# Kernel optimization log

Hardware: AMD Instinct MI355X
Metric: run time of the kernel (lower is better)

The kernel has to match this reference:

```python
import jax, jax.numpy as jnp
import numpy as np

ALPHA = 0.2  # LeakyReLU negative slope


def setup_inputs() -> dict:
    key = jax.random.key(0)
    k1, k2, k3, k4 = jax.random.split(key, 4)
    B, N, F_in, F_out = 2, 512, 256, 128
    x = jax.random.normal(k1, (B, N, F_in), dtype=jnp.float32)
    adj = jax.random.randint(k2, (B, N, N), 0, 2, dtype=jnp.int32)
    # xavier_uniform with gain=1.414 for W (in_features, out_features)
    limit = 1.414 * np.sqrt(6.0 / (F_in + F_out))
    W = jax.random.uniform(k3, (F_in, F_out), dtype=jnp.float32, minval=-limit, maxval=limit)
    # attn_fc: Linear(out_features, 1, bias=False); store its weight as a vector
    lim_a = np.sqrt(1.0 / F_out)
    a_fc = jax.random.uniform(k4, (F_out,), dtype=jnp.float32, minval=-lim_a, maxval=lim_a)
    return {"x": x, "adj": adj, "W": W, "a_fc": a_fc}


def reference(x, adj, W, a_fc):
    # x: [B,N,F_in], adj: [B,N,N], W: [F_in,F_out], a_fc: [F_out]
    Wh = jnp.einsum('bnf,fo->bno', x, W)                         # [B,N,O]
    s = Wh[:, :, None, :] + Wh[:, None, :, :]                    # [B,N,N,O] broadcast concat-sum
    e = jnp.einsum('bijo,o->bij', jax.nn.leaky_relu(s, ALPHA), a_fc)  # attn_fc -> [B,N,N]
    e = e / jnp.sqrt(jnp.sum(e * e))                             # torch.linalg.norm over whole tensor
    e = jnp.where(adj == 0, -jnp.inf, e)
    attention = jax.nn.softmax(e, axis=-1)
    h_prime = jnp.einsum('bij,bjo->bio', attention, Wh)          # [B,N,O]
    return jax.nn.elu(h_prime)                                   # concat=True -> elu
```

## Files before the change

kernel.cpp:

```cpp
#include <hip/hip_runtime.h>
#include <math.h>

constexpr int BB   = 2;
constexpr int NN   = 512;
constexpr int FIN  = 256;
constexpr int FOUT = 128;

__global__ __launch_bounds__(512) void wh_u_kernel(const float* __restrict__ x,
                                                   const float* __restrict__ W,
                                                   const float* __restrict__ a_fc,
                                                   float* __restrict__ Wh,
                                                   float* __restrict__ u) {
    __shared__ float  xs[4][FIN];
    __shared__ float4 part[4][4][32];
    __shared__ float  upart[8][4];

    const int t  = threadIdx.x;
    const int g0 = blockIdx.x * 4;

    if (t < 256)
        ((float4*)xs)[t] = ((const float4*)(x + (size_t)g0 * FIN))[t];
    __syncthreads();

    const int rl = t >> 7;
    const int fs = (t >> 5) & 3;
    const int og = t & 31;
    const float* xr = &xs[rl][fs * 64];
    const float4* W4 = (const float4*)W;

    float4 acc = {0.f, 0.f, 0.f, 0.f};
#pragma unroll 8
    for (int f = 0; f < 64; ++f) {
        const float  xv = xr[f];
        const float4 wv = W4[(size_t)(fs * 64 + f) * 32 + og];
        acc.x = fmaf(xv, wv.x, acc.x);
        acc.y = fmaf(xv, wv.y, acc.y);
        acc.z = fmaf(xv, wv.z, acc.z);
        acc.w = fmaf(xv, wv.w, acc.w);
    }
    part[rl][fs][og] = acc;
    __syncthreads();

    if (t < 128) {
        const int crl = t & 3;
        const int cog = t >> 2;
        const float4 s0 = part[crl][0][cog];
        const float4 s1 = part[crl][1][cog];
        const float4 s2 = part[crl][2][cog];
        const float4 s3 = part[crl][3][cog];
        float4 w4;
        w4.x = (s0.x + s1.x) + (s2.x + s3.x);
        w4.y = (s0.y + s1.y) + (s2.y + s3.y);
        w4.z = (s0.z + s1.z) + (s2.z + s3.z);
        w4.w = (s0.w + s1.w) + (s2.w + s3.w);
        ((float4*)(Wh + (size_t)(g0 + crl) * FOUT))[cog] = w4;

        const float4 a4 = ((const float4*)a_fc)[cog];
        float pa = w4.x * a4.x + w4.y * a4.y + w4.z * a4.z + w4.w * a4.w;
#pragma unroll
        for (int off = 32; off >= 4; off >>= 1) pa += __shfl_down(pa, off);
        if ((t & 63) < 4) upart[t >> 6][t & 3] = pa;
    }
    __syncthreads();
    if (t < 4) {
        u[g0 + t] = upart[0][t] + upart[1][t];
    }
}

__global__ __launch_bounds__(256) void e_kernel(const float* __restrict__ Wh,
                                                const float* __restrict__ u,
                                                const float* __restrict__ a_fc,
                                                float* __restrict__ e_buf,
                                                float* __restrict__ partials) {
    __shared__ float whi[32][132];
    __shared__ float whj[16][132];
    __shared__ float a2[FOUT];
    __shared__ float usi[32];
    __shared__ float usj[16];
    __shared__ float parts[16][4][33];
    __shared__ float red[4];

    const int t   = threadIdx.x;
    const int bj0 = blockIdx.x * 16;
    const int bi0 = blockIdx.y * 32;
    const int b   = blockIdx.z;
    const float* whb = Wh + (size_t)(b * NN) * FOUT;

#pragma unroll
    for (int it = 0; it < 4; ++it) {
        const int idx = it * 256 + t;
        const int row = idx >> 5, c4 = idx & 31;
        *(float4*)&whi[row][c4 * 4] =
            *(const float4*)(whb + (size_t)(bi0 + row) * FOUT + c4 * 4);
    }
#pragma unroll
    for (int it = 0; it < 2; ++it) {
        const int idx = it * 256 + t;
        const int row = idx >> 5, c4 = idx & 31;
        *(float4*)&whj[row][c4 * 4] =
            *(const float4*)(whb + (size_t)(bj0 + row) * FOUT + c4 * 4);
    }
    if (t < 32)            usi[t]       = u[b * NN + bi0 + t];
    else if (t < 48)       usj[t - 32]  = u[b * NN + bj0 + (t - 32)];
    else if (t >= 128)     a2[t - 128]  = 0.4f * a_fc[t - 128];
    __syncthreads();

    const int w    = t >> 6;
    const int lane = t & 63;
    const int i    = lane & 31;
    const int jh   = lane >> 5;
    const int ob   = w * 32;

    float4 iv[8], av[8];
#pragma unroll
    for (int k = 0; k < 8; ++k) {
        iv[k] = *(const float4*)&whi[i][ob + 4 * k];
        av[k] = *(const float4*)&a2[ob + 4 * k];
    }

#pragma unroll
    for (int jj = 0; jj < 8; ++jj) {
        const int j = jh * 8 + jj;
        float4 acc = {0.f, 0.f, 0.f, 0.f};
#pragma unroll
        for (int k = 0; k < 8; ++k) {
            const float4 jv = *(const float4*)&whj[j][ob + 4 * k];
            float s;
            s = iv[k].x + jv.x; acc.x = fmaf(av[k].x, fabsf(s), acc.x);
            s = iv[k].y + jv.y; acc.y = fmaf(av[k].y, fabsf(s), acc.y);
            s = iv[k].z + jv.z; acc.z = fmaf(av[k].z, fabsf(s), acc.z);
            s = iv[k].w + jv.w; acc.w = fmaf(av[k].w, fabsf(s), acc.w);
        }
        parts[j][w][i] = (acc.x + acc.y) + (acc.z + acc.w);
    }
    __syncthreads();

    const int ci = t >> 3;
    const int jp = (t & 7) * 2;
    const float ui = usi[ci];

    const float S0 = (parts[jp][0][ci] + parts[jp][1][ci]) +
                     (parts[jp][2][ci] + parts[jp][3][ci]);
    const float v0 = fmaf(0.6f, ui + usj[jp], S0);
    const float S1 = (parts[jp + 1][0][ci] + parts[jp + 1][1][ci]) +
                     (parts[jp + 1][2][ci] + parts[jp + 1][3][ci]);
    const float v1 = fmaf(0.6f, ui + usj[jp + 1], S1);
    float ss = fmaf(v0, v0, v1 * v1);

    float2 e2 = {v0, v1};
    *(float2*)&e_buf[(size_t)(b * NN + bi0 + ci) * NN + bj0 + jp] = e2;

#pragma unroll
    for (int off = 32; off; off >>= 1) ss += __shfl_down(ss, off);
    if ((t & 63) == 0) red[t >> 6] = ss;
    __syncthreads();
    if (t == 0)
        partials[(blockIdx.z * 16 + blockIdx.y) * 32 + blockIdx.x] =
            (red[0] + red[1]) + (red[2] + red[3]);
}

__global__ __launch_bounds__(256) void softmax_pv_kernel(
        const float* __restrict__ e_buf, const int* __restrict__ adj,
        const float* __restrict__ Wh, const float* __restrict__ partials,
        float* __restrict__ out) {
    __shared__ float p[4][NN];
    __shared__ float hb[3][4][64];
    __shared__ float red[4];
    __shared__ float rsv[4];

    const int t    = threadIdx.x;
    const int w    = t >> 6;
    const int lane = t & 63;

    float v = (partials[t] + partials[t + 256]) +
              (partials[t + 512] + partials[t + 768]);
#pragma unroll
    for (int off = 32; off; off >>= 1) v += __shfl_down(v, off);
    if (lane == 0) red[w] = v;
    __syncthreads();
    const float inv_norm = 1.0f / sqrtf((red[0] + red[1]) + (red[2] + red[3]));

    const int g0  = (blockIdx.x & 255) * 4;
    const int row = g0 + w;

    const float4* er4 = (const float4*)(e_buf + (size_t)row * NN);
    const int4*   ad4 = (const int4*)(adj + (size_t)row * NN);
    const float4 ea = er4[lane],     eb = er4[lane + 64];
    const int4   aa = ad4[lane],     ab = ad4[lane + 64];

    float va[8];
    va[0] = aa.x ? ea.x * inv_norm : -INFINITY;
    va[1] = aa.y ? ea.y * inv_norm : -INFINITY;
    va[2] = aa.z ? ea.z * inv_norm : -INFINITY;
    va[3] = aa.w ? ea.w * inv_norm : -INFINITY;
    va[4] = ab.x ? eb.x * inv_norm : -INFINITY;
    va[5] = ab.y ? eb.y * inv_norm : -INFINITY;
    va[6] = ab.z ? eb.z * inv_norm : -INFINITY;
    va[7] = ab.w ? eb.w * inv_norm : -INFINITY;

    float mx = va[0];
#pragma unroll
    for (int c = 1; c < 8; ++c) mx = fmaxf(mx, va[c]);
#pragma unroll
    for (int off = 32; off; off >>= 1) mx = fmaxf(mx, __shfl_xor(mx, off));

    float pv[8], sum = 0.f;
#pragma unroll
    for (int c = 0; c < 8; ++c) { pv[c] = expf(va[c] - mx); sum += pv[c]; }
    float4 pa = {pv[0], pv[1], pv[2], pv[3]};
    float4 pb = {pv[4], pv[5], pv[6], pv[7]};
    ((float4*)&p[w][0])[lane]      = pa;
    ((float4*)&p[w][0])[lane + 64] = pb;

#pragma unroll
    for (int off = 32; off; off >>= 1) sum += __shfl_xor(sum, off);
    if (lane == 0) rsv[w] = 1.0f / sum;
    __syncthreads();

    const int oo = lane;
    const int o  = (blockIdx.x >> 8) * 64 + oo;
    const int b  = g0 >> 9;
    const float* whb = Wh + (size_t)(b * NN) * FOUT;
    const int j0 = w * 128;

    float acc[4] = {0.f, 0.f, 0.f, 0.f};
    for (int j = j0; j < j0 + 128; j += 4) {
        const float4 p0 = *(const float4*)&p[0][j];
        const float4 p1 = *(const float4*)&p[1][j];
        const float4 p2 = *(const float4*)&p[2][j];
        const float4 p3 = *(const float4*)&p[3][j];
        const float q0[4] = {p0.x, p0.y, p0.z, p0.w};
        const float q1[4] = {p1.x, p1.y, p1.z, p1.w};
        const float q2[4] = {p2.x, p2.y, p2.z, p2.w};
        const float q3[4] = {p3.x, p3.y, p3.z, p3.w};
#pragma unroll
        for (int q = 0; q < 4; ++q) {
            const float wv = whb[(size_t)(j + q) * FOUT + o];
            acc[0] = fmaf(q0[q], wv, acc[0]);
            acc[1] = fmaf(q1[q], wv, acc[1]);
            acc[2] = fmaf(q2[q], wv, acc[2]);
            acc[3] = fmaf(q3[q], wv, acc[3]);
        }
    }

    if (w) {
        hb[w - 1][0][oo] = acc[0];
        hb[w - 1][1][oo] = acc[1];
        hb[w - 1][2][oo] = acc[2];
        hb[w - 1][3][oo] = acc[3];
    }
    __syncthreads();
    if (w == 0) {
#pragma unroll
        for (int r = 0; r < 4; ++r) {
            const float hv = (acc[r] + hb[0][r][oo] + hb[1][r][oo] + hb[2][r][oo]) * rsv[r];
            out[(size_t)(g0 + r) * FOUT + o] = (hv > 0.f) ? hv : expm1f(hv);
        }
    }
}

extern "C" void kernel_launch(void* const* d_in, const int* in_sizes, int n_in,
                              void* d_out, int out_size, void* d_ws, size_t ws_size,
                              hipStream_t stream) {
    const float* x    = (const float*)d_in[0];
    const int*   adj  = (const int*)d_in[1];
    const float* W    = (const float*)d_in[2];
    const float* a_fc = (const float*)d_in[3];
    float* out = (float*)d_out;

    float* ws       = (float*)d_ws;
    float* Wh       = ws;
    float* u        = ws + 131072;
    float* partials = ws + 131072 + 1024;
    float* e_buf    = ws + 131072 + 2048;

    wh_u_kernel<<<dim3(BB * NN / 4), dim3(512), 0, stream>>>(x, W, a_fc, Wh, u);
    e_kernel<<<dim3(NN / 16, NN / 32, BB), dim3(256), 0, stream>>>(Wh, u, a_fc, e_buf, partials);
    softmax_pv_kernel<<<dim3(512), dim3(256), 0, stream>>>(e_buf, adj, Wh, partials, out);
}
```

Measured before the change: 25.78 us.

## Repartition Wh projection and softmax-PV work across more, smaller thread blocks

The Wh/u projection kernel now runs 512 blocks of 256 threads. Each block handles two rows, split into eight 32-wide feature slices, and each thread computes both rows so every W load is reused twice. The softmax-PV kernel now launches 1024 blocks, each covering 32 output columns instead of 64, and splits the j-reduction into eight 64-wide chunks that are combined in shared memory. The aim is higher occupancy and more parallelism on the GPU. In exchange, the softmax prologue (reading e_buf and adj rows, max/exp/sum) is now recomputed four times per row instead of twice.

```diff
diff --git a/kernel.cpp b/kernel.cpp
--- a/kernel.cpp
+++ b/kernel.cpp
@@ -6,64 +6,62 @@
 constexpr int FIN  = 256;
 constexpr int FOUT = 128;
 
-__global__ __launch_bounds__(512) void wh_u_kernel(const float* __restrict__ x,
+__global__ __launch_bounds__(256) void wh_u_kernel(const float* __restrict__ x,
                                                    const float* __restrict__ W,
                                                    const float* __restrict__ a_fc,
                                                    float* __restrict__ Wh,
                                                    float* __restrict__ u) {
-    __shared__ float  xs[4][FIN];
-    __shared__ float4 part[4][4][32];
-    __shared__ float  upart[8][4];
+    __shared__ float  xs[2][FIN];
+    __shared__ float4 part[2][8][32];
 
     const int t  = threadIdx.x;
-    const int g0 = blockIdx.x * 4;
-
-    if (t < 256)
+    const int g0 = blockIdx.x * 2;
+
+    if (t < 128)
         ((float4*)xs)[t] = ((const float4*)(x + (size_t)g0 * FIN))[t];
     __syncthreads();
 
-    const int rl = t >> 7;
-    const int fs = (t >> 5) & 3;
+    const int fs = t >> 5;
     const int og = t & 31;
-    const float* xr = &xs[rl][fs * 64];
+    const float* x0 = &xs[0][fs * 32];
+    const float* x1 = &xs[1][fs * 32];
     const float4* W4 = (const float4*)W;
 
-    float4 acc = {0.f, 0.f, 0.f, 0.f};
+    float4 a0 = {0.f, 0.f, 0.f, 0.f};
+    float4 a1 = {0.f, 0.f, 0.f, 0.f};
 #pragma unroll 8
-    for (int f = 0; f < 64; ++f) {
-        const float  xv = xr[f];
-        const float4 wv = W4[(size_t)(fs * 64 + f) * 32 + og];
-        acc.x = fmaf(xv, wv.x, acc.x);
-        acc.y = fmaf(xv, wv.y, acc.y);
-        acc.z = fmaf(xv, wv.z, acc.z);
-        acc.w = fmaf(xv, wv.w, acc.w);
-    }
-    part[rl][fs][og] = acc;
-    __syncthreads();
-
-    if (t < 128) {
-        const int crl = t & 3;
-        const int cog = t >> 2;
-        const float4 s0 = part[crl][0][cog];
-        const float4 s1 = part[crl][1][cog];
-        const float4 s2 = part[crl][2][cog];
-        const float4 s3 = part[crl][3][cog];
+    for (int f = 0; f < 32; ++f) {
+        const float4 wv = W4[(size_t)(fs * 32 + f) * 32 + og];
+        const float v0 = x0[f];
+        const float v1 = x1[f];
+        a0.x = fmaf(v0, wv.x, a0.x); a1.x = fmaf(v1, wv.x, a1.x);
+        a0.y = fmaf(v0, wv.y, a0.y); a1.y = fmaf(v1, wv.y, a1.y);
+        a0.z = fmaf(v0, wv.z, a0.z); a1.z = fmaf(v1, wv.z, a1.z);
+        a0.w = fmaf(v0, wv.w, a0.w); a1.w = fmaf(v1, wv.w, a1.w);
+    }
+    part[0][fs][og] = a0;
+    part[1][fs][og] = a1;
+    __syncthreads();
+
+    if (t < 64) {
+        const int rl = t >> 5;
+        const int o4 = t & 31;
+        float4 s0 = part[rl][0][o4], s1 = part[rl][1][o4];
+        float4 s2 = part[rl][2][o4], s3 = part[rl][3][o4];
+        float4 s4 = part[rl][4][o4], s5 = part[rl][5][o4];
+        float4 s6 = part[rl][6][o4], s7 = part[rl][7][o4];
         float4 w4;
-        w4.x = (s0.x + s1.x) + (s2.x + s3.x);
-        w4.y = (s0.y + s1.y) + (s2.y + s3.y);
-        w4.z = (s0.z + s1.z) + (s2.z + s3.z);
-        w4.w = (s0.w + s1.w) + (s2.w + s3.w);
-        ((float4*)(Wh + (size_t)(g0 + crl) * FOUT))[cog] = w4;
-
-        const float4 a4 = ((const float4*)a_fc)[cog];
+        w4.x = ((s0.x + s1.x) + (s2.x + s3.x)) + ((s4.x + s5.x) + (s6.x + s7.x));
+        w4.y = ((s0.y + s1.y) + (s2.y + s3.y)) + ((s4.y + s5.y) + (s6.y + s7.y));
+        w4.z = ((s0.z + s1.z) + (s2.z + s3.z)) + ((s4.z + s5.z) + (s6.z + s7.z));
+        w4.w = ((s0.w + s1.w) + (s2.w + s3.w)) + ((s4.w + s5.w) + (s6.w + s7.w));
+        ((float4*)(Wh + (size_t)(g0 + rl) * FOUT))[o4] = w4;
+
+        const float4 a4 = ((const float4*)a_fc)[o4];
         float pa = w4.x * a4.x + w4.y * a4.y + w4.z * a4.z + w4.w * a4.w;
 #pragma unroll
-        for (int off = 32; off >= 4; off >>= 1) pa += __shfl_down(pa, off);
-        if ((t & 63) < 4) upart[t >> 6][t & 3] = pa;
-    }
-    __syncthreads();
-    if (t < 4) {
-        u[g0 + t] = upart[0][t] + upart[1][t];
+        for (int off = 16; off; off >>= 1) pa += __shfl_down(pa, off, 32);
+        if (o4 == 0) u[g0 + rl] = pa;
     }
 }
 
@@ -164,7 +162,7 @@
         const float* __restrict__ Wh, const float* __restrict__ partials,
         float* __restrict__ out) {
     __shared__ float p[4][NN];
-    __shared__ float hb[3][4][64];
+    __shared__ float hb[8][4][32];
     __shared__ float red[4];
     __shared__ float rsv[4];
 
@@ -181,6 +179,7 @@
     const float inv_norm = 1.0f / sqrtf((red[0] + red[1]) + (red[2] + red[3]));
 
     const int g0  = (blockIdx.x & 255) * 4;
+    const int oq  = blockIdx.x >> 8;
     const int row = g0 + w;
 
     const float4* er4 = (const float4*)(e_buf + (size_t)row * NN);
@@ -217,45 +216,47 @@
     if (lane == 0) rsv[w] = 1.0f / sum;
     __syncthreads();
 
-    const int oo = lane;
-    const int o  = (blockIdx.x >> 8) * 64 + oo;
+    const int oo = lane & 31;
+    const int o  = oq * 32 + oo;
+    const int jc = (w << 1) | (lane >> 5);
     const int b  = g0 >> 9;
     const float* whb = Wh + (size_t)(b * NN) * FOUT;
-    const int j0 = w * 128;
-
-    float acc[4] = {0.f, 0.f, 0.f, 0.f};
-    for (int j = j0; j < j0 + 128; j += 4) {
+    const int j0 = jc * 64;
+
+    float acc0 = 0.f, acc1 = 0.f, acc2 = 0.f, acc3 = 0.f;
+    for (int j = j0; j < j0 + 64; j += 4) {
         const float4 p0 = *(const float4*)&p[0][j];
         const float4 p1 = *(const float4*)&p[1][j];
         const float4 p2 = *(const float4*)&p[2][j];
         const float4 p3 = *(const float4*)&p[3][j];
-        const float q0[4] = {p0.x, p0.y, p0.z, p0.w};
-        const float q1[4] = {p1.x, p1.y, p1.z, p1.w};
-        const float q2[4] = {p2.x, p2.y, p2.z, p2.w};
-        const float q3[4] = {p3.x, p3.y, p3.z, p3.w};
-#pragma unroll
-        for (int q = 0; q < 4; ++q) {
-            const float wv = whb[(size_t)(j + q) * FOUT + o];
-            acc[0] = fmaf(q0[q], wv, acc[0]);
-            acc[1] = fmaf(q1[q], wv, acc[1]);
-            acc[2] = fmaf(q2[q], wv, acc[2]);
-            acc[3] = fmaf(q3[q], wv, acc[3]);
-        }
-    }
-
-    if (w) {
-        hb[w - 1][0][oo] = acc[0];
-        hb[w - 1][1][oo] = acc[1];
-        hb[w - 1][2][oo] = acc[2];
-        hb[w - 1][3][oo] = acc[3];
-    }
-    __syncthreads();
-    if (w == 0) {
-#pragma unroll
-        for (int r = 0; r < 4; ++r) {
-            const float hv = (acc[r] + hb[0][r][oo] + hb[1][r][oo] + hb[2][r][oo]) * rsv[r];
-            out[(size_t)(g0 + r) * FOUT + o] = (hv > 0.f) ? hv : expm1f(hv);
-        }
+        float wv;
+        wv = whb[(size_t)(j + 0) * FOUT + o];
+        acc0 = fmaf(p0.x, wv, acc0); acc1 = fmaf(p1.x, wv, acc1);
+        acc2 = fmaf(p2.x, wv, acc2); acc3 = fmaf(p3.x, wv, acc3);
+        wv = whb[(size_t)(j + 1) * FOUT + o];
+        acc0 = fmaf(p0.y, wv, acc0); acc1 = fmaf(p1.y, wv, acc1);
+        acc2 = fmaf(p2.y, wv, acc2); acc3 = fmaf(p3.y, wv, acc3);
+        wv = whb[(size_t)(j + 2) * FOUT + o];
+        acc0 = fmaf(p0.z, wv, acc0); acc1 = fmaf(p1.z, wv, acc1);
+        acc2 = fmaf(p2.z, wv, acc2); acc3 = fmaf(p3.z, wv, acc3);
+        wv = whb[(size_t)(j + 3) * FOUT + o];
+        acc0 = fmaf(p0.w, wv, acc0); acc1 = fmaf(p1.w, wv, acc1);
+        acc2 = fmaf(p2.w, wv, acc2); acc3 = fmaf(p3.w, wv, acc3);
+    }
+
+    hb[jc][0][oo] = acc0;
+    hb[jc][1][oo] = acc1;
+    hb[jc][2][oo] = acc2;
+    hb[jc][3][oo] = acc3;
+    __syncthreads();
+
+    if (t < 128) {
+        const int r  = t >> 5;
+        const int o2 = t & 31;
+        float h = ((hb[0][r][o2] + hb[1][r][o2]) + (hb[2][r][o2] + hb[3][r][o2])) +
+                  ((hb[4][r][o2] + hb[5][r][o2]) + (hb[6][r][o2] + hb[7][r][o2]));
+        h *= rsv[r];
+        out[(size_t)(g0 + r) * FOUT + oq * 32 + o2] = (h > 0.f) ? h : expm1f(h);
     }
 }
 
@@ -274,7 +275,7 @@
     float* partials = ws + 131072 + 1024;
     float* e_buf    = ws + 131072 + 2048;
 
-    wh_u_kernel<<<dim3(BB * NN / 4), dim3(512), 0, stream>>>(x, W, a_fc, Wh, u);
+    wh_u_kernel<<<dim3(BB * NN / 2), dim3(256), 0, stream>>>(x, W, a_fc, Wh, u);
     e_kernel<<<dim3(NN / 16, NN / 32, BB), dim3(256), 0, stream>>>(Wh, u, a_fc, e_buf, partials);
-    softmax_pv_kernel<<<dim3(512), dim3(256), 0, stream>>>(e_buf, adj, Wh, partials, out);
-}
+    softmax_pv_kernel<<<dim3(1024), dim3(256), 0, stream>>>(e_buf, adj, Wh, partials, out);
+}
```

New measurement: 25.26 us. 1.02x faster.
